# Optimization experiments

Hardware: AMD Instinct MI355X
Metric: run time of the kernel (lower is better)

The kernel has to match this reference:

```python
import jax, jax.numpy as jnp
import numpy as np

N = 50000   # nodes
E = 800000  # edges
F = 128     # input features
H = 128     # hidden channels
G = 64      # graphs in batch
C = 10      # classes
L_HID = 3   # residual hidden GCN blocks
EPS = 1e-5  # BatchNorm eps


def setup_inputs() -> dict:
    key = jax.random.key(0)
    ks = jax.random.split(key, 10)
    sc = lambda k, s: (jax.random.normal(k, s, jnp.float32) * 0.05)
    x = jax.random.normal(ks[0], (N, F), jnp.float32)
    edge_index = jax.random.randint(ks[1], (2, E), 0, N, dtype=jnp.int32)
    batch = jnp.sort(jax.random.randint(ks[2], (N,), 0, G, dtype=jnp.int32))
    return {
        "x": x, "edge_index": edge_index, "batch": batch,
        # initial GCN block
        "W0": sc(ks[3], (F, H)), "b0": jnp.zeros(H, jnp.float32),
        "g0": jnp.ones(H, jnp.float32), "be0": jnp.zeros(H, jnp.float32),
        # 3 residual GCN blocks (stacked)
        "Wh": sc(ks[4], (L_HID, H, H)), "bh": jnp.zeros((L_HID, H), jnp.float32),
        "gh": jnp.ones((L_HID, H), jnp.float32), "beh": jnp.zeros((L_HID, H), jnp.float32),
        "Rh": sc(ks[5], (L_HID, H, H)),  # residual Linear (no bias)
        # MLP head: Linear(H,H)+ReLU, Linear(H,C)
        "mW1": sc(ks[6], (H, H)), "mb1": jnp.zeros(H, jnp.float32),
        "mW2": sc(ks[7], (H, C)), "mb2": jnp.zeros(C, jnp.float32),
    }


def _gcn_norm(edge_index, n):
    # add self-loops + symmetric normalization, as in PyG GCNConv
    loop = jnp.arange(n, dtype=edge_index.dtype)
    src = jnp.concatenate([edge_index[0], loop])
    dst = jnp.concatenate([edge_index[1], loop])
    deg = jax.ops.segment_sum(jnp.ones_like(dst, jnp.float32), dst, num_segments=n)
    dinv = jnp.where(deg > 0, jax.lax.rsqrt(deg), 0.0)
    coef = dinv[src] * dinv[dst]  # [E+N]
    return src, dst, coef


def _gcn_conv(x, W, b, src, dst, coef, n):
    h = x @ W                                   # [N, H] linear first (PyG order)
    msg = h[src] * coef[:, None]                # gather + normalize  [E+N, H]
    agg = jax.ops.segment_sum(msg, dst, num_segments=n)  # scatter-add [N, H]
    return agg + b


def _bn_relu(h, gamma, beta):
    # BatchNorm1d in eval mode with running_mean=0, running_var=1
    inv = jax.lax.rsqrt(jnp.asarray(1.0 + EPS, h.dtype))
    return jax.nn.relu(h * inv * gamma + beta)  # dropout is identity in eval


def reference(x, edge_index, batch, W0, b0, g0, be0, Wh, bh, gh, beh, Rh, mW1, mb1, mW2, mb2):
    n = x.shape[0]
    src, dst, coef = _gcn_norm(edge_index, n)
    # initial block (no residual)
    h = _bn_relu(_gcn_conv(x, W0, b0, src, dst, coef, n), g0, be0)
    # residual hidden blocks
    for i in range(Wh.shape[0]):
        c = _gcn_conv(h, Wh[i], bh[i], src, dst, coef, n) + h @ Rh[i]
        h = _bn_relu(c, gh[i], beh[i])
    # global max pool over graphs in the batch
    pooled = jax.ops.segment_max(h, batch, num_segments=G)  # [G, H]
    # MLP head
    z = jax.nn.relu(pooled @ mW1 + mb1)
    return z @ mW2 + mb2  # [G, C]
```

## Files before the change

kernel.cpp:

```cpp
#include <hip/hip_runtime.h>
#include <cstdint>
#include <cstddef>

#define NN 50000
#define NE 800000
#define NEPAD (NE + 3 * NN)
#define HID 128
#define NGRAPH 64
#define NCLASS 10
#define LHID 3

#define ROWBLK 3125
#define ROWBLK_PAD 3128
#define GEMM_GRID 782
#define FILL_GRID 3125
#define FRONT_A 3125
#define FRONT_B 56
#define FRONT_GRID (FRONT_A + FRONT_B + 3125)

static constexpr float BN_INV = 0.9999950000374996f;

typedef __attribute__((ext_vector_type(8))) __bf16 bf16x8;
typedef __attribute__((ext_vector_type(4))) float floatx4;


__device__ __forceinline__ unsigned int f32_to_bf16_rne(float f) {
    unsigned int u = __float_as_uint(f);
    return (u + 0x7FFFu + ((u >> 16) & 1u)) >> 16;
}
__device__ __forceinline__ float bf16_to_f32(unsigned int h) {
    return __uint_as_float(h << 16);
}
__device__ __forceinline__ void split2(float a, float b, unsigned int& hi,
                                       unsigned int& lo) {
    unsigned int h0 = f32_to_bf16_rne(a), h1 = f32_to_bf16_rne(b);
    unsigned int l0 = f32_to_bf16_rne(a - bf16_to_f32(h0));
    unsigned int l1 = f32_to_bf16_rne(b - bf16_to_f32(h1));
    hi = h0 | (h1 << 16);
    lo = l0 | (l1 << 16);
}

__device__ __forceinline__ void gl2lds16(const void* g, void* l) {
    __builtin_amdgcn_global_load_lds((__attribute__((address_space(1))) void*)g,
                                     (__attribute__((address_space(3))) void*)l,
                                     16, 0, 0);
}


__global__ void k_front(const float* __restrict__ x, unsigned short* __restrict__ xH,
                        unsigned short* __restrict__ xL,
                        const float* __restrict__ W0, const float* __restrict__ Wh,
                        const float* __restrict__ Rh, unsigned short* __restrict__ bH,
                        unsigned short* __restrict__ bL,
                        const int* __restrict__ ei, int* __restrict__ deg,
                        int* __restrict__ eslot) {
    const int b = blockIdx.x;
    const int tid = threadIdx.x;
    if (b < FRONT_A) {
        int u = b * 256 + tid;
        int lane = u & 63;
        int blk = u >> 6;
        int kblk = blk & 3;
        int rowBlock = blk >> 2;
        int m = rowBlock * 16 + (lane & 15);
        int k = kblk * 32 + (lane >> 4) * 8;
        const float4* p = (const float4*)&x[(size_t)m * 128 + k];
        float4 v0 = p[0];
        float4 v1 = p[1];
        float vals[8] = {v0.x, v0.y, v0.z, v0.w, v1.x, v1.y, v1.z, v1.w};
        union { unsigned int i[4]; uint4 v; } H, L;
#pragma unroll
        for (int j = 0; j < 4; ++j) split2(vals[2 * j], vals[2 * j + 1], H.i[j], L.i[j]);
        *(uint4*)&xH[(size_t)u * 8] = H.v;
        *(uint4*)&xL[(size_t)u * 8] = L.v;
    } else if (b < FRONT_A + FRONT_B) {
        int cb = b - FRONT_A;
        int mat = cb >> 3;
        const float* src = (mat == 0) ? W0
                         : (mat <= 3) ? (Wh + (size_t)(mat - 1) * 16384)
                                      : (Rh + (size_t)(mat - 4) * 16384);
        int u = (cb & 7) * 256 + tid;
        int lane = u & 63;
        int blk = u >> 6;
        int kblk = blk & 3;
        int nb = blk >> 2;
        int n = nb * 16 + (lane & 15);
        int k = kblk * 32 + (lane >> 4) * 8;
        union { unsigned int i[4]; uint4 v; } H, L;
#pragma unroll
        for (int j = 0; j < 4; ++j) {
            float a = src[(size_t)(k + 2 * j) * 128 + n];
            float c = src[(size_t)(k + 2 * j + 1) * 128 + n];
            split2(a, c, H.i[j], L.i[j]);
        }
        size_t base = (size_t)mat * 16384 + (size_t)u * 8;
        *(uint4*)&bH[base] = H.v;
        *(uint4*)&bL[base] = L.v;
    } else {
        int e = (b - FRONT_A - FRONT_B) * 256 + tid;
        int d = ei[NE + e];
        eslot[e] = atomicAdd(&deg[d], 1);
    }
}


__global__ void k_scan1(const int* __restrict__ deg, float* __restrict__ dinv,
                        int* __restrict__ bsum) {
    __shared__ int s[256];
    int i = blockIdx.x * 256 + threadIdx.x;
    int d = (i < NN) ? deg[i] : 0;
    if (i < NN) dinv[i] = rsqrtf((float)(d + 1));
    s[threadIdx.x] = (d + 3) & ~3;
    __syncthreads();
    for (int o = 128; o > 0; o >>= 1) {
        if (threadIdx.x < o) s[threadIdx.x] += s[threadIdx.x + o];
        __syncthreads();
    }
    if (threadIdx.x == 0) bsum[blockIdx.x] = s[0];
}


__global__ void k_scan3(const int* __restrict__ deg, const int* __restrict__ bsum,
                        int* __restrict__ rowptr, int* __restrict__ col,
                        float* __restrict__ cfv) {
    __shared__ int s[256];
    __shared__ int offS;
    const int bid = blockIdx.x;
    s[threadIdx.x] = (threadIdx.x < bid) ? bsum[threadIdx.x] : 0;
    __syncthreads();
    for (int o = 128; o > 0; o >>= 1) {
        if (threadIdx.x < o) s[threadIdx.x] += s[threadIdx.x + o];
        __syncthreads();
    }
    if (threadIdx.x == 0) offS = s[0];
    __syncthreads();
    const int off = offS;
    __syncthreads();
    int i = bid * 256 + threadIdx.x;
    int d = (i < NN) ? deg[i] : 0;
    int v = (d + 3) & ~3;
    s[threadIdx.x] = v;
    __syncthreads();
    for (int o = 1; o < 256; o <<= 1) {
        int tv = (threadIdx.x >= o) ? s[threadIdx.x - o] : 0;
        __syncthreads();
        s[threadIdx.x] += tv;
        __syncthreads();
    }
    if (i < NN) {
        int rp = off + s[threadIdx.x] - v;
        rowptr[i] = rp;
        for (int p = rp + d; p < rp + v; ++p) { col[p] = 0; cfv[p] = 0.f; }
    }
}


template <int NB, bool FILL>
__global__ __launch_bounds__(256, 3) void k_gemm_mfma(
    const unsigned short* __restrict__ Ahi, const unsigned short* __restrict__ Alo,
    const unsigned short* __restrict__ B1hi, const unsigned short* __restrict__ B1lo,
    const unsigned short* __restrict__ B2hi, const unsigned short* __restrict__ B2lo,
    float* __restrict__ C1, float* __restrict__ C2,
    const int* __restrict__ ei, const int* __restrict__ rowptr,
    const int* __restrict__ eslot, const float* __restrict__ dinv,
    int* __restrict__ col, float* __restrict__ cfv) {
    __shared__ unsigned short lds[(1 + 2 * NB) * 4096];
    if (FILL && blockIdx.x >= GEMM_GRID) {
        int e = (blockIdx.x - GEMM_GRID) * 256 + threadIdx.x;
        int s = ei[e];
        int d = ei[NE + e];
        int p = rowptr[d] + eslot[e];
        col[p] = s;
        cfv[p] = dinv[s];
        return;
    }
    unsigned short* AhiS = lds;
    unsigned short* AloS = lds + 2048;
    unsigned short* B1hiS = lds + 4096;
    unsigned short* B1loS = lds + 8192;
    unsigned short* B2hiS = lds + 12288;
    unsigned short* B2loS = lds + 16384;

    const int tid = threadIdx.x;
    const int wave = tid >> 6;
    const int lane = tid & 63;
    const int wm = wave & 1;
    const int wn = wave >> 1;
    const int rb0 = blockIdx.x * 4;

    floatx4 acc1[2][4], acc2[2][4];
    floatx4 zero = {0.f, 0.f, 0.f, 0.f};
#pragma unroll
    for (int i = 0; i < 2; ++i)
#pragma unroll
        for (int j = 0; j < 4; ++j) { acc1[i][j] = zero; if (NB == 2) acc2[i][j] = zero; }

    for (int kc = 0; kc < 4; ++kc) {
        const int nit = (NB == 2) ? 10 : 6;
#pragma unroll
        for (int it = 0; it < nit; ++it) {
            int i = it * 4 + wave;
            const unsigned short* src;
            unsigned short* dst;
            if (i < 4)       { src = Ahi  + ((size_t)(rb0 + i) * 4 + kc) * 512;       dst = AhiS  + i * 512; }
            else if (i < 8)  { int rb = i - 4;  src = Alo  + ((size_t)(rb0 + rb) * 4 + kc) * 512; dst = AloS  + rb * 512; }
            else if (i < 16) { int nb = i - 8;  src = B1hi + ((size_t)nb * 4 + kc) * 512;         dst = B1hiS + nb * 512; }
            else if (i < 24) { int nb = i - 16; src = B1lo + ((size_t)nb * 4 + kc) * 512;         dst = B1loS + nb * 512; }
            else if (i < 32) { int nb = i - 24; src = B2hi + ((size_t)nb * 4 + kc) * 512;         dst = B2hiS + nb * 512; }
            else             { int nb = i - 32; src = B2lo + ((size_t)nb * 4 + kc) * 512;         dst = B2loS + nb * 512; }
            gl2lds16(src + (size_t)lane * 8, dst);
        }
        __syncthreads();

        bf16x8 aH[2], aL[2], bH[4], bL[4];
#pragma unroll
        for (int t = 0; t < 2; ++t)
            aH[t] = *(const bf16x8*)(AhiS + (wm * 2 + t) * 512 + lane * 8);
#pragma unroll
        for (int t = 0; t < 4; ++t)
            bH[t] = *(const bf16x8*)(B1hiS + (wn * 4 + t) * 512 + lane * 8);
#pragma unroll
        for (int tm = 0; tm < 2; ++tm)
#pragma unroll
            for (int tn = 0; tn < 4; ++tn)
                acc1[tm][tn] = __builtin_amdgcn_mfma_f32_16x16x32_bf16(
                    aH[tm], bH[tn], acc1[tm][tn], 0, 0, 0);
#pragma unroll
        for (int t = 0; t < 4; ++t)
            bL[t] = *(const bf16x8*)(B1loS + (wn * 4 + t) * 512 + lane * 8);
#pragma unroll
        for (int tm = 0; tm < 2; ++tm)
#pragma unroll
            for (int tn = 0; tn < 4; ++tn)
                acc1[tm][tn] = __builtin_amdgcn_mfma_f32_16x16x32_bf16(
                    aH[tm], bL[tn], acc1[tm][tn], 0, 0, 0);
#pragma unroll
        for (int t = 0; t < 2; ++t)
            aL[t] = *(const bf16x8*)(AloS + (wm * 2 + t) * 512 + lane * 8);
#pragma unroll
        for (int tm = 0; tm < 2; ++tm)
#pragma unroll
            for (int tn = 0; tn < 4; ++tn)
                acc1[tm][tn] = __builtin_amdgcn_mfma_f32_16x16x32_bf16(
                    aL[tm], bH[tn], acc1[tm][tn], 0, 0, 0);
        if (NB == 2) {
#pragma unroll
            for (int t = 0; t < 4; ++t)
                bH[t] = *(const bf16x8*)(B2hiS + (wn * 4 + t) * 512 + lane * 8);
#pragma unroll
            for (int tm = 0; tm < 2; ++tm)
#pragma unroll
                for (int tn = 0; tn < 4; ++tn)
                    acc2[tm][tn] = __builtin_amdgcn_mfma_f32_16x16x32_bf16(
                        aH[tm], bH[tn], acc2[tm][tn], 0, 0, 0);
#pragma unroll
            for (int tm = 0; tm < 2; ++tm)
#pragma unroll
                for (int tn = 0; tn < 4; ++tn)
                    acc2[tm][tn] = __builtin_amdgcn_mfma_f32_16x16x32_bf16(
                        aL[tm], bH[tn], acc2[tm][tn], 0, 0, 0);
#pragma unroll
            for (int t = 0; t < 4; ++t)
                bL[t] = *(const bf16x8*)(B2loS + (wn * 4 + t) * 512 + lane * 8);
#pragma unroll
            for (int tm = 0; tm < 2; ++tm)
#pragma unroll
                for (int tn = 0; tn < 4; ++tn)
                    acc2[tm][tn] = __builtin_amdgcn_mfma_f32_16x16x32_bf16(
                        aH[tm], bL[tn], acc2[tm][tn], 0, 0, 0);
        }
        __syncthreads();
    }

    const int quad = lane >> 4;
    const int col0 = lane & 15;
    const int rowBase = blockIdx.x * 64 + wm * 32;
#pragma unroll
    for (int tm = 0; tm < 2; ++tm) {
#pragma unroll
        for (int tn = 0; tn < 4; ++tn) {
            int c = wn * 64 + tn * 16 + col0;
#pragma unroll
            for (int r = 0; r < 4; ++r) {
                int row = rowBase + tm * 16 + quad * 4 + r;
                if (row < NN) {
                    C1[(size_t)row * 128 + c] = acc1[tm][tn][r];
                    if (NB == 2) C2[(size_t)row * 128 + c] = acc2[tm][tn][r];
                }
            }
        }
    }
}


template <bool RES, bool LAST>
__global__ __launch_bounds__(1024) void k_spmm(const float* __restrict__ t,
                                               const float* __restrict__ r,
                                               const int* __restrict__ rowptr,
                                               const int* __restrict__ deg,
                                               const int* __restrict__ col,
                                               const float* __restrict__ cfv,
                                               const float* __restrict__ dinv,
                                               const float* __restrict__ bias,
                                               const float* __restrict__ gamma,
                                               const float* __restrict__ beta,
                                               unsigned short* __restrict__ hHi,
                                               unsigned short* __restrict__ hLo,
                                               const int* __restrict__ batch,
                                               float* __restrict__ pooled) {
    __shared__ unsigned short shH[16][136];
    __shared__ unsigned short shL[16][136];
    __shared__ float shP[16][64][2];
    const int lane = threadIdx.x & 63;
    const int wave = threadIdx.x >> 6;
    const int f = lane * 2;
    const int node = blockIdx.x * 16 + wave;

    const float2 bv = *(const float2*)&bias[f];
    const float2 gv = *(const float2*)&gamma[f];
    const float2 ev = *(const float2*)&beta[f];

    const int start = rowptr[node];
    const int cnt4 = (deg[node] + 3) >> 2;
    float ax = 0.f, ay = 0.f;
#pragma unroll 2
    for (int q = 0; q < cnt4; ++q) {
        int4 cs = *(const int4*)&col[start + q * 4];
        float4 wv = *(const float4*)&cfv[start + q * 4];
        float2 v0 = *(const float2*)&t[(size_t)cs.x * 128 + f];
        float2 v1 = *(const float2*)&t[(size_t)cs.y * 128 + f];
        float2 v2 = *(const float2*)&t[(size_t)cs.z * 128 + f];
        float2 v3 = *(const float2*)&t[(size_t)cs.w * 128 + f];
        ax = fmaf(wv.x, v0.x, ax); ay = fmaf(wv.x, v0.y, ay);
        ax = fmaf(wv.y, v1.x, ax); ay = fmaf(wv.y, v1.y, ay);
        ax = fmaf(wv.z, v2.x, ax); ay = fmaf(wv.z, v2.y, ay);
        ax = fmaf(wv.w, v3.x, ax); ay = fmaf(wv.w, v3.y, ay);
    }
    const float di = dinv[node];
    const float dii = di * di;
    float2 tv = *(const float2*)&t[(size_t)node * 128 + f];
    float cx = di * ax + dii * tv.x + bv.x;
    float cy = di * ay + dii * tv.y + bv.y;
    if (RES) {
        float2 rv = *(const float2*)&r[(size_t)node * 128 + f];
        cx += rv.x;
        cy += rv.y;
    }
    const float ox = fmaxf(cx * (BN_INV * gv.x) + ev.x, 0.f);
    const float oy = fmaxf(cy * (BN_INV * gv.y) + ev.y, 0.f);

    if (LAST) {
        bool uni = (batch[blockIdx.x * 16] == batch[blockIdx.x * 16 + 15]);
        if (uni) {
            shP[wave][lane][0] = ox;
            shP[wave][lane][1] = oy;
            __syncthreads();
            if (wave == 0) {
                float a = shP[0][lane][0], b = shP[0][lane][1];
#pragma unroll
                for (int w = 1; w < 16; ++w) {
                    a = fmaxf(a, shP[w][lane][0]);
                    b = fmaxf(b, shP[w][lane][1]);
                }
                int g = batch[blockIdx.x * 16];
                atomicMax((unsigned int*)&pooled[g * 128 + f], __float_as_uint(a));
                atomicMax((unsigned int*)&pooled[g * 128 + f + 1], __float_as_uint(b));
            }
        } else {
            int g = batch[node];
            atomicMax((unsigned int*)&pooled[g * 128 + f], __float_as_uint(ox));
            atomicMax((unsigned int*)&pooled[g * 128 + f + 1], __float_as_uint(oy));
        }
        return;
    }

    unsigned int H, L;
    split2(ox, oy, H, L);
    ((unsigned int*)&shH[wave][0])[lane] = H;
    ((unsigned int*)&shL[wave][0])[lane] = L;
    __syncthreads();

    const int u = threadIdx.x >> 6;
    const int l = threadIdx.x & 63;
    const int m = l & 15;
    const int kg = l >> 4;
    if (u < 4) {
        uint4 H4 = *(const uint4*)&shH[m][u * 32 + kg * 8];
        ((uint4*)hHi)[((size_t)blockIdx.x * 4 + u) * 64 + l] = H4;
    } else if (u < 8) {
        int uu = u - 4;
        uint4 L4 = *(const uint4*)&shL[m][uu * 32 + kg * 8];
        ((uint4*)hLo)[((size_t)blockIdx.x * 4 + uu) * 64 + l] = L4;
    }
}


__global__ void k_head(const float* __restrict__ pooled, const float* __restrict__ mW1,
                       const float* __restrict__ mb1, const float* __restrict__ mW2,
                       const float* __restrict__ mb2, float* __restrict__ out) {
    __shared__ float p[128];
    __shared__ float z[128];
    int g = blockIdx.x;
    int j = threadIdx.x;
    p[j] = pooled[g * 128 + j];
    __syncthreads();
    float a = mb1[j];
#pragma unroll 8
    for (int k = 0; k < 128; ++k) a += p[k] * mW1[k * 128 + j];
    z[j] = fmaxf(a, 0.f);
    __syncthreads();
    if (j < NCLASS) {
        float o = mb2[j];
#pragma unroll 8
        for (int k = 0; k < 128; ++k) o += z[k] * mW2[k * NCLASS + j];
        out[g * NCLASS + j] = o;
    }
}


extern "C" void kernel_launch(void* const* d_in, const int* in_sizes, int n_in,
                              void* d_out, int out_size, void* d_ws, size_t ws_size,
                              hipStream_t stream) {
    const float* x   = (const float*)d_in[0];
    const int*   ei  = (const int*)d_in[1];
    const int* batch = (const int*)d_in[2];
    const float* W0  = (const float*)d_in[3];
    const float* b0  = (const float*)d_in[4];
    const float* g0  = (const float*)d_in[5];
    const float* be0 = (const float*)d_in[6];
    const float* Wh  = (const float*)d_in[7];
    const float* bh  = (const float*)d_in[8];
    const float* gh  = (const float*)d_in[9];
    const float* beh = (const float*)d_in[10];
    const float* Rh  = (const float*)d_in[11];
    const float* mW1 = (const float*)d_in[12];
    const float* mb1 = (const float*)d_in[13];
    const float* mW2 = (const float*)d_in[14];
    const float* mb2 = (const float*)d_in[15];
    float* out = (float*)d_out;

    char* ws = (char*)d_ws;
    size_t off = 0;
    auto alloc = [&](size_t bytes) -> void* {
        void* p = ws + off;
        off += (bytes + 255) & ~(size_t)255;
        return p;
    };
    int*   deg    = (int*)alloc((size_t)NN * 4);
    float* pooled = (float*)alloc((size_t)NGRAPH * HID * 4);
    size_t zspan = (size_t)((char*)pooled - (char*)deg) + (size_t)NGRAPH * HID * 4;
    int*   rowptr = (int*)alloc((size_t)NN * 4);
    float* dinv   = (float*)alloc((size_t)NN * 4);
    int*   bsum   = (int*)alloc(256 * 4);
    int*   eslot  = (int*)alloc((size_t)NE * 4);
    int*   col    = (int*)alloc((size_t)NEPAD * 4);
    float* cfv    = (float*)alloc((size_t)NEPAD * 4);
    float* t      = (float*)alloc((size_t)NN * HID * 4);
    float* rbuf   = (float*)alloc((size_t)NN * HID * 4);
    const size_t ASZ = (size_t)ROWBLK_PAD * 4 * 512;
    unsigned short* xH = (unsigned short*)alloc(ASZ * 2);
    unsigned short* xL = (unsigned short*)alloc(ASZ * 2);
    unsigned short* hH0 = (unsigned short*)alloc(ASZ * 2);
    unsigned short* hL0 = (unsigned short*)alloc(ASZ * 2);
    unsigned short* hH1 = (unsigned short*)alloc(ASZ * 2);
    unsigned short* hL1 = (unsigned short*)alloc(ASZ * 2);
    unsigned short* bH = (unsigned short*)alloc((size_t)7 * 16384 * 2);
    unsigned short* bL = (unsigned short*)alloc((size_t)7 * 16384 * 2);

    hipMemsetAsync(deg, 0, zspan, stream);

    k_front<<<FRONT_GRID, 256, 0, stream>>>(x, xH, xL, W0, Wh, Rh, bH, bL,
                                            ei, deg, eslot);
    k_scan1<<<(NN + 255) / 256, 256, 0, stream>>>(deg, dinv, bsum);
    k_scan3<<<(NN + 255) / 256, 256, 0, stream>>>(deg, bsum, rowptr, col, cfv);

    k_gemm_mfma<1, true><<<GEMM_GRID + FILL_GRID, 256, 0, stream>>>(
        xH, xL, bH, bL, nullptr, nullptr, t, nullptr,
        ei, rowptr, eslot, dinv, col, cfv);

    const int spmmGrid = NN / 16;
    k_spmm<false, false><<<spmmGrid, 1024, 0, stream>>>(
        t, nullptr, rowptr, deg, col, cfv, dinv, b0, g0, be0, hH0, hL0,
        nullptr, nullptr);

    unsigned short* hh[2] = {hH0, hH1};
    unsigned short* hl[2] = {hL0, hL1};
    int cur = 0;
    for (int i = 0; i < LHID; ++i) {
        unsigned short* ih = hh[cur];
        unsigned short* il = hl[cur];
        unsigned short* oh = hh[cur ^ 1];
        unsigned short* ol = hl[cur ^ 1];
        const unsigned short* w1H = bH + (size_t)(1 + i) * 16384;
        const unsigned short* w1L = bL + (size_t)(1 + i) * 16384;
        const unsigned short* w2H = bH + (size_t)(4 + i) * 16384;
        const unsigned short* w2L = bL + (size_t)(4 + i) * 16384;
        k_gemm_mfma<2, false><<<GEMM_GRID, 256, 0, stream>>>(
            ih, il, w1H, w1L, w2H, w2L, t, rbuf,
            nullptr, nullptr, nullptr, nullptr, nullptr, nullptr);
        if (i < LHID - 1)
            k_spmm<true, false><<<spmmGrid, 1024, 0, stream>>>(
                t, rbuf, rowptr, deg, col, cfv, dinv, bh + i * HID, gh + i * HID,
                beh + i * HID, oh, ol, nullptr, nullptr);
        else
            k_spmm<true, true><<<spmmGrid, 1024, 0, stream>>>(
                t, rbuf, rowptr, deg, col, cfv, dinv, bh + i * HID, gh + i * HID,
                beh + i * HID, nullptr, nullptr, batch, pooled);
        cur ^= 1;
    }

    k_head<<<NGRAPH, 128, 0, stream>>>(pooled, mW1, mb1, mW2, mb2, out);
}
```

Measured before the change: 509.5 us.

## Replicate degree counters across 8 copies and interleave CSR column/weight pairs

Degree counting now spreads atomics over 8 replicated counter arrays chosen by edge index, which is meant to reduce atomic contention on popular destination nodes. The scan kernel then computes per-replica offsets. The CSR column index and coefficient arrays are merged into one int2 pairs array, so SpMM loads index and weight together. The degree block is also moved to the front of the launch grid. In exchange, the memset gets larger and there is an extra degOff array read during the CSR fill.

```diff
diff --git a/kernel.cpp b/kernel.cpp
--- a/kernel.cpp
+++ b/kernel.cpp
@@ -9,14 +9,16 @@
 #define NGRAPH 64
 #define NCLASS 10
 #define LHID 3
+#define NREP 8
 
 #define ROWBLK 3125
 #define ROWBLK_PAD 3128
 #define GEMM_GRID 782
 #define FILL_GRID 3125
+#define FRONT_DEG 3125
 #define FRONT_A 3125
 #define FRONT_B 56
-#define FRONT_GRID (FRONT_A + FRONT_B + 3125)
+#define FRONT_GRID (FRONT_DEG + FRONT_A + FRONT_B)
 
 static constexpr float BN_INV = 0.9999950000374996f;
 
@@ -52,12 +54,17 @@
                         const float* __restrict__ W0, const float* __restrict__ Wh,
                         const float* __restrict__ Rh, unsigned short* __restrict__ bH,
                         unsigned short* __restrict__ bL,
-                        const int* __restrict__ ei, int* __restrict__ deg,
+                        const int* __restrict__ ei, int* __restrict__ deg8,
                         int* __restrict__ eslot) {
     const int b = blockIdx.x;
     const int tid = threadIdx.x;
-    if (b < FRONT_A) {
-        int u = b * 256 + tid;
+    if (b < FRONT_DEG) {
+        int e = b * 256 + tid;
+        int d = ei[NE + e];
+        int rep = e & (NREP - 1);
+        eslot[e] = atomicAdd(&deg8[rep * NN + d], 1);
+    } else if (b < FRONT_DEG + FRONT_A) {
+        int u = (b - FRONT_DEG) * 256 + tid;
         int lane = u & 63;
         int blk = u >> 6;
         int kblk = blk & 3;
@@ -73,8 +80,8 @@
         for (int j = 0; j < 4; ++j) split2(vals[2 * j], vals[2 * j + 1], H.i[j], L.i[j]);
         *(uint4*)&xH[(size_t)u * 8] = H.v;
         *(uint4*)&xL[(size_t)u * 8] = L.v;
-    } else if (b < FRONT_A + FRONT_B) {
-        int cb = b - FRONT_A;
+    } else {
+        int cb = b - FRONT_DEG - FRONT_A;
         int mat = cb >> 3;
         const float* src = (mat == 0) ? W0
                          : (mat <= 3) ? (Wh + (size_t)(mat - 1) * 16384)
@@ -96,21 +103,29 @@
         size_t base = (size_t)mat * 16384 + (size_t)u * 8;
         *(uint4*)&bH[base] = H.v;
         *(uint4*)&bL[base] = L.v;
-    } else {
-        int e = (b - FRONT_A - FRONT_B) * 256 + tid;
-        int d = ei[NE + e];
-        eslot[e] = atomicAdd(&deg[d], 1);
-    }
-}
-
-
-__global__ void k_scan1(const int* __restrict__ deg, float* __restrict__ dinv,
+    }
+}
+
+
+__global__ void k_scan1(const int* __restrict__ deg8, int* __restrict__ degT,
+                        int* __restrict__ degOff, float* __restrict__ dinv,
                         int* __restrict__ bsum) {
     __shared__ int s[256];
     int i = blockIdx.x * 256 + threadIdx.x;
-    int d = (i < NN) ? deg[i] : 0;
-    if (i < NN) dinv[i] = rsqrtf((float)(d + 1));
-    s[threadIdx.x] = (d + 3) & ~3;
+    int dsum = 0;
+    if (i < NN) {
+        int off[NREP];
+#pragma unroll
+        for (int r = 0; r < NREP; ++r) {
+            off[r] = dsum;
+            dsum += deg8[r * NN + i];
+        }
+#pragma unroll
+        for (int r = 0; r < NREP; ++r) degOff[i * NREP + r] = off[r];
+        degT[i] = dsum;
+        dinv[i] = rsqrtf((float)(dsum + 1));
+    }
+    s[threadIdx.x] = (dsum + 3) & ~3;
     __syncthreads();
     for (int o = 128; o > 0; o >>= 1) {
         if (threadIdx.x < o) s[threadIdx.x] += s[threadIdx.x + o];
@@ -120,9 +135,8 @@
 }
 
 
-__global__ void k_scan3(const int* __restrict__ deg, const int* __restrict__ bsum,
-                        int* __restrict__ rowptr, int* __restrict__ col,
-                        float* __restrict__ cfv) {
+__global__ void k_scan3(const int* __restrict__ degT, const int* __restrict__ bsum,
+                        int* __restrict__ rowptr, int2* __restrict__ pairs) {
     __shared__ int s[256];
     __shared__ int offS;
     const int bid = blockIdx.x;
@@ -137,7 +151,7 @@
     const int off = offS;
     __syncthreads();
     int i = bid * 256 + threadIdx.x;
-    int d = (i < NN) ? deg[i] : 0;
+    int d = (i < NN) ? degT[i] : 0;
     int v = (d + 3) & ~3;
     s[threadIdx.x] = v;
     __syncthreads();
@@ -150,7 +164,7 @@
     if (i < NN) {
         int rp = off + s[threadIdx.x] - v;
         rowptr[i] = rp;
-        for (int p = rp + d; p < rp + v; ++p) { col[p] = 0; cfv[p] = 0.f; }
+        for (int p = rp + d; p < rp + v; ++p) pairs[p] = make_int2(0, 0);
     }
 }
 
@@ -162,16 +176,16 @@
     const unsigned short* __restrict__ B2hi, const unsigned short* __restrict__ B2lo,
     float* __restrict__ C1, float* __restrict__ C2,
     const int* __restrict__ ei, const int* __restrict__ rowptr,
-    const int* __restrict__ eslot, const float* __restrict__ dinv,
-    int* __restrict__ col, float* __restrict__ cfv) {
+    const int* __restrict__ eslot, const int* __restrict__ degOff,
+    const float* __restrict__ dinv, int2* __restrict__ pairs) {
     __shared__ unsigned short lds[(1 + 2 * NB) * 4096];
     if (FILL && blockIdx.x >= GEMM_GRID) {
         int e = (blockIdx.x - GEMM_GRID) * 256 + threadIdx.x;
         int s = ei[e];
         int d = ei[NE + e];
-        int p = rowptr[d] + eslot[e];
-        col[p] = s;
-        cfv[p] = dinv[s];
+        int rep = e & (NREP - 1);
+        int p = rowptr[d] + degOff[d * NREP + rep] + eslot[e];
+        pairs[p] = make_int2(s, __float_as_int(dinv[s]));
         return;
     }
     unsigned short* AhiS = lds;
@@ -297,9 +311,8 @@
 __global__ __launch_bounds__(1024) void k_spmm(const float* __restrict__ t,
                                                const float* __restrict__ r,
                                                const int* __restrict__ rowptr,
-                                               const int* __restrict__ deg,
-                                               const int* __restrict__ col,
-                                               const float* __restrict__ cfv,
+                                               const int* __restrict__ degT,
+                                               const int2* __restrict__ pairs,
                                                const float* __restrict__ dinv,
                                                const float* __restrict__ bias,
                                                const float* __restrict__ gamma,
@@ -321,20 +334,22 @@
     const float2 ev = *(const float2*)&beta[f];
 
     const int start = rowptr[node];
-    const int cnt4 = (deg[node] + 3) >> 2;
+    const int cnt4 = (degT[node] + 3) >> 2;
     float ax = 0.f, ay = 0.f;
 #pragma unroll 2
     for (int q = 0; q < cnt4; ++q) {
-        int4 cs = *(const int4*)&col[start + q * 4];
-        float4 wv = *(const float4*)&cfv[start + q * 4];
-        float2 v0 = *(const float2*)&t[(size_t)cs.x * 128 + f];
-        float2 v1 = *(const float2*)&t[(size_t)cs.y * 128 + f];
-        float2 v2 = *(const float2*)&t[(size_t)cs.z * 128 + f];
-        float2 v3 = *(const float2*)&t[(size_t)cs.w * 128 + f];
-        ax = fmaf(wv.x, v0.x, ax); ay = fmaf(wv.x, v0.y, ay);
-        ax = fmaf(wv.y, v1.x, ax); ay = fmaf(wv.y, v1.y, ay);
-        ax = fmaf(wv.z, v2.x, ax); ay = fmaf(wv.z, v2.y, ay);
-        ax = fmaf(wv.w, v3.x, ax); ay = fmaf(wv.w, v3.y, ay);
+        int4 p0 = *(const int4*)&pairs[start + q * 4];
+        int4 p1 = *(const int4*)&pairs[start + q * 4 + 2];
+        float2 v0 = *(const float2*)&t[(size_t)p0.x * 128 + f];
+        float2 v1 = *(const float2*)&t[(size_t)p0.z * 128 + f];
+        float2 v2 = *(const float2*)&t[(size_t)p1.x * 128 + f];
+        float2 v3 = *(const float2*)&t[(size_t)p1.z * 128 + f];
+        float w0 = __int_as_float(p0.y), w1 = __int_as_float(p0.w);
+        float w2 = __int_as_float(p1.y), w3 = __int_as_float(p1.w);
+        ax = fmaf(w0, v0.x, ax); ay = fmaf(w0, v0.y, ay);
+        ax = fmaf(w1, v1.x, ax); ay = fmaf(w1, v1.y, ay);
+        ax = fmaf(w2, v2.x, ax); ay = fmaf(w2, v2.y, ay);
+        ax = fmaf(w3, v3.x, ax); ay = fmaf(w3, v3.y, ay);
     }
     const float di = dinv[node];
     const float dii = di * di;
@@ -446,15 +461,16 @@
         off += (bytes + 255) & ~(size_t)255;
         return p;
     };
-    int*   deg    = (int*)alloc((size_t)NN * 4);
+    int*   deg8   = (int*)alloc((size_t)NREP * NN * 4);
     float* pooled = (float*)alloc((size_t)NGRAPH * HID * 4);
-    size_t zspan = (size_t)((char*)pooled - (char*)deg) + (size_t)NGRAPH * HID * 4;
+    size_t zspan = (size_t)((char*)pooled - (char*)deg8) + (size_t)NGRAPH * HID * 4;
+    int*   degT   = (int*)alloc((size_t)NN * 4);
+    int*   degOff = (int*)alloc((size_t)NN * NREP * 4);
     int*   rowptr = (int*)alloc((size_t)NN * 4);
     float* dinv   = (float*)alloc((size_t)NN * 4);
     int*   bsum   = (int*)alloc(256 * 4);
     int*   eslot  = (int*)alloc((size_t)NE * 4);
-    int*   col    = (int*)alloc((size_t)NEPAD * 4);
-    float* cfv    = (float*)alloc((size_t)NEPAD * 4);
+    int2*  pairs  = (int2*)alloc((size_t)NEPAD * 8);
     float* t      = (float*)alloc((size_t)NN * HID * 4);
     float* rbuf   = (float*)alloc((size_t)NN * HID * 4);
     const size_t ASZ = (size_t)ROWBLK_PAD * 4 * 512;
@@ -467,20 +483,20 @@
     unsigned short* bH = (unsigned short*)alloc((size_t)7 * 16384 * 2);
     unsigned short* bL = (unsigned short*)alloc((size_t)7 * 16384 * 2);
 
-    hipMemsetAsync(deg, 0, zspan, stream);
+    hipMemsetAsync(deg8, 0, zspan, stream);
 
     k_front<<<FRONT_GRID, 256, 0, stream>>>(x, xH, xL, W0, Wh, Rh, bH, bL,
-                                            ei, deg, eslot);
-    k_scan1<<<(NN + 255) / 256, 256, 0, stream>>>(deg, dinv, bsum);
-    k_scan3<<<(NN + 255) / 256, 256, 0, stream>>>(deg, bsum, rowptr, col, cfv);
+                                            ei, deg8, eslot);
+    k_scan1<<<(NN + 255) / 256, 256, 0, stream>>>(deg8, degT, degOff, dinv, bsum);
+    k_scan3<<<(NN + 255) / 256, 256, 0, stream>>>(degT, bsum, rowptr, pairs);
 
     k_gemm_mfma<1, true><<<GEMM_GRID + FILL_GRID, 256, 0, stream>>>(
         xH, xL, bH, bL, nullptr, nullptr, t, nullptr,
-        ei, rowptr, eslot, dinv, col, cfv);
+        ei, rowptr, eslot, degOff, dinv, pairs);
 
     const int spmmGrid = NN / 16;
     k_spmm<false, false><<<spmmGrid, 1024, 0, stream>>>(
-        t, nullptr, rowptr, deg, col, cfv, dinv, b0, g0, be0, hH0, hL0,
+        t, nullptr, rowptr, degT, pairs, dinv, b0, g0, be0, hH0, hL0,
         nullptr, nullptr);
 
     unsigned short* hh[2] = {hH0, hH1};
@@ -500,11 +516,11 @@
             nullptr, nullptr, nullptr, nullptr, nullptr, nullptr);
         if (i < LHID - 1)
             k_spmm<true, false><<<spmmGrid, 1024, 0, stream>>>(
-                t, rbuf, rowptr, deg, col, cfv, dinv, bh + i * HID, gh + i * HID,
+                t, rbuf, rowptr, degT, pairs, dinv, bh + i * HID, gh + i * HID,
                 beh + i * HID, oh, ol, nullptr, nullptr);
         else
             k_spmm<true, true><<<spmmGrid, 1024, 0, stream>>>(
-                t, rbuf, rowptr, deg, col, cfv, dinv, bh + i * HID, gh + i * HID,
+                t, rbuf, rowptr, degT, pairs, dinv, bh + i * HID, gh + i * HID,
                 beh + i * HID, nullptr, nullptr, batch, pooled);
         cur ^= 1;
     }
```

Result: slower. 558.6 us (+9.6%).
